# Performance work log

Measured on AMD Instinct MI355X. Metric: run time of the kernel, lower is better.

Reference implementation:

```python
import jax, jax.numpy as jnp
import numpy as np

S, B, D, H, F = 4096, 2, 512, 8, 2048
Dh = D // H
EPS = 1e-5


def _rotate_half(x):
    # matches torch: cat((-x[..., 1::2], x[..., ::2]), dim=-1)
    return jnp.concatenate([-x[..., 1::2], x[..., ::2]], axis=-1)


def _layer_norm(x, w, b):
    m = jnp.mean(x, axis=-1, keepdims=True)
    v = jnp.mean(jnp.square(x - m), axis=-1, keepdims=True)
    return (x - m) * jax.lax.rsqrt(v + EPS) * w + b


def setup_inputs() -> dict:
    key = jax.random.key(0)
    ks = jax.random.split(key, 6)
    p = lambda k, shape: (jax.random.normal(k, shape, jnp.float32) * 0.02)
    src = jax.random.normal(ks[0], (S, B, D), jnp.float32)
    # standard RoPE tables, broadcastable to [S, B, H, Dh]
    pos = jnp.arange(S, dtype=jnp.float32)
    inv_freq = 1.0 / (10000.0 ** (jnp.arange(0, Dh, 2, dtype=jnp.float32) / Dh))
    ang = pos[:, None] * inv_freq[None, :]          # [S, Dh/2]
    emb = jnp.concatenate([ang, ang], axis=-1)       # [S, Dh]
    rotary_cos = jnp.cos(emb)[:, None, None, :]
    rotary_sin = jnp.sin(emb)[:, None, None, :]
    return {
        "src": src,
        "rotary_cos": rotary_cos,
        "rotary_sin": rotary_sin,
        "in_proj_w": p(ks[1], (3 * D, D)),
        "in_proj_b": jnp.zeros((3 * D,), jnp.float32),
        "out_proj_w": p(ks[2], (D, D)),
        "out_proj_b": jnp.zeros((D,), jnp.float32),
        "w1": p(ks[3], (F, D)),
        "b1": jnp.zeros((F,), jnp.float32),
        "w2": p(ks[4], (D, F)),
        "b2": jnp.zeros((D,), jnp.float32),
        "ln1_w": jnp.ones((D,), jnp.float32),
        "ln1_b": jnp.zeros((D,), jnp.float32),
        "ln2_w": jnp.ones((D,), jnp.float32),
        "ln2_b": jnp.zeros((D,), jnp.float32),
    }


def reference(src, rotary_cos, rotary_sin, in_proj_w, in_proj_b,
              out_proj_w, out_proj_b, w1, b1, w2, b2,
              ln1_w, ln1_b, ln2_w, ln2_b):
    s = src.shape[0]
    x = _layer_norm(src, ln1_w, ln1_b)                       # [S,B,D]
    # RoPE on pre-projection tensor (q_s == k_s == x reshaped)
    xs = x.reshape(s, B, H, Dh)
    xr = (xs * rotary_cos + _rotate_half(xs) * rotary_sin).reshape(s, B, D)
    # MultiheadAttention packed in-projection
    wq, wk, wv = jnp.split(in_proj_w, 3, axis=0)
    bq, bk, bv = jnp.split(in_proj_b, 3, axis=0)
    q = (xr @ wq.T + bq).reshape(s, B, H, Dh)
    k = (xr @ wk.T + bk).reshape(s, B, H, Dh)
    v = (x @ wv.T + bv).reshape(s, B, H, Dh)
    scale = 1.0 / np.sqrt(Dh).astype(np.float32)
    scores = jnp.einsum('sbhd,tbhd->bhst', q, k) * scale     # [B,H,S,S]
    causal = jnp.triu(jnp.ones((s, s), dtype=bool), k=1)     # True = masked
    scores = jnp.where(causal, -jnp.inf, scores)
    probs = jax.nn.softmax(scores, axis=-1)
    attn = jnp.einsum('bhst,tbhd->sbhd', probs, v).reshape(s, B, D)
    attn = attn @ out_proj_w.T + out_proj_b
    src = src + attn                                         # dropout=identity (eval)
    # GELU FFN (exact erf, torch nn.GELU default)
    y = _layer_norm(src, ln2_w, ln2_b)
    y = jax.nn.gelu(y @ w1.T + b1, approximate=False) @ w2.T + b2
    return src + y
```

## Files before the change

kernel.cpp:

```cpp
#include <hip/hip_runtime.h>
#include <hip/hip_bf16.h>

typedef unsigned short u16;
typedef unsigned int u32;
using short8 = __attribute__((ext_vector_type(8))) short;
using f32x4  = __attribute__((ext_vector_type(4))) float;
using f32x16 = __attribute__((ext_vector_type(16))) float;

#define MFMA16(a,b,c) __builtin_amdgcn_mfma_f32_16x16x32_bf16((a),(b),(c),0,0,0)
#define MFMA32(a,b,c) __builtin_amdgcn_mfma_f32_32x32x16_bf16((a),(b),(c),0,0,0)
#define EXP2F(x) __builtin_amdgcn_exp2f(x)

__device__ __forceinline__ float bf2f(u16 u){
  union { u32 i; float f; } v; v.i = ((u32)u)<<16; return v.f;
}
__device__ __forceinline__ u16 f2bf(float f){
  u32 x = __float_as_uint(f);
  x += 0x7fffu + ((x>>16)&1u);
  return (u16)(x>>16);
}
__device__ __forceinline__ u32 cvtpk(float lo, float hi){
  u32 r;
  asm("v_cvt_pk_bf16_f32 %0, %1, %2" : "=v"(r) : "v"(lo), "v"(hi));
  return r;
}
__device__ __forceinline__ float cross_max(float v){
  u32 b = __float_as_uint(v);
  auto r = __builtin_amdgcn_permlane32_swap(b, b, false, false);
  return fmaxf(__uint_as_float(r[0]), __uint_as_float(r[1]));
}
__device__ __forceinline__ float cross_sum(float v){
  u32 b = __float_as_uint(v);
  auto r = __builtin_amdgcn_permlane32_swap(b, b, false, false);
  return __uint_as_float(r[0]) + __uint_as_float(r[1]);
}

typedef __attribute__((address_space(1))) const u32 GU32;
typedef __attribute__((address_space(3))) u32 LU32;
typedef __attribute__((address_space(3))) const u16 LDSU16C;
__device__ __forceinline__ void gload_lds16(const void* g, void* l){
  __builtin_amdgcn_global_load_lds((GU32*)g, (LU32*)l, 16, 0, 0);
}

template<int OFF>
__device__ __forceinline__ uint2 tr16(const u16* p){
  uint2 r;
  if constexpr (OFF == 0)
    asm volatile("ds_read_b64_tr_b16 %0, %1" : "=v"(r) : "v"((LDSU16C*)p));
  else
    asm volatile("ds_read_b64_tr_b16 %0, %1 offset:128" : "=v"(r) : "v"((LDSU16C*)p));
  return r;
}

struct ConvArgs {
  const float4* in[14];
  uint2* out[14];
  int n4[14];
  int sb[15];
};
__global__ __launch_bounds__(256)
void conv_all(ConvArgs a)
{
  int bid = blockIdx.x;
  int s = 0;
  while (s < 13 && bid >= a.sb[s+1]) ++s;
  int i = (bid - a.sb[s])*256 + threadIdx.x;
  if (i >= a.n4[s]) return;
  float4 v = a.in[s][i];
  union { uint2 u; u16 h[4]; } o;
  o.h[0] = f2bf(v.x); o.h[1] = f2bf(v.y);
  o.h[2] = f2bf(v.z); o.h[3] = f2bf(v.w);
  a.out[s][i] = o.u;
}

template<int DO_ROPE, int IN_F32>
__global__ __launch_bounds__(256)
void ln_kernel(const void* __restrict__ inv, const u16* __restrict__ lw,
               const u16* __restrict__ lb, const u16* __restrict__ ct,
               const u16* __restrict__ st, u16* __restrict__ xo,
               u16* __restrict__ xro)
{
  __shared__ float xs[4][512];
  int tid = threadIdx.x, wid = tid>>6, lane = tid&63;
  int m = blockIdx.x*4 + wid;
  int d0 = lane*8;
  float v[8], sum = 0.f, sq = 0.f;
  if (IN_F32){
    const float* in = (const float*)inv;
    float4 a = *(const float4*)(in + (size_t)m*512 + d0);
    float4 b = *(const float4*)(in + (size_t)m*512 + d0 + 4);
    v[0]=a.x; v[1]=a.y; v[2]=a.z; v[3]=a.w;
    v[4]=b.x; v[5]=b.y; v[6]=b.z; v[7]=b.w;
  } else {
    const u16* in = (const u16*)inv;
    union { uint4 q; u16 s[8]; } pk;
    pk.q = *(const uint4*)(in + (size_t)m*512 + d0);
#pragma unroll
    for (int j=0;j<8;j++) v[j] = bf2f(pk.s[j]);
  }
#pragma unroll
  for (int j=0;j<8;j++){ sum+=v[j]; sq+=v[j]*v[j]; }
#pragma unroll
  for (int o=1;o<64;o<<=1){ sum += __shfl_xor(sum,o); sq += __shfl_xor(sq,o); }
  float mean = sum*(1.f/512.f);
  float var  = sq*(1.f/512.f) - mean*mean;
  float rstd = rsqrtf(var + 1e-5f);
  float xn[8];
  union { uint4 q; u16 s[8]; } ou;
#pragma unroll
  for (int j=0;j<8;j++){
    int d = d0+j;
    xn[j] = (v[j]-mean)*rstd*bf2f(lw[d]) + bf2f(lb[d]);
    ou.s[j] = f2bf(xn[j]);
  }
  *(uint4*)(xo + (size_t)m*512 + d0) = ou.q;
  if (DO_ROPE){
#pragma unroll
    for (int j=0;j<8;j++) xs[wid][d0+j] = xn[j];
    __syncthreads();
    int si = m>>1;
    int hb = d0 & ~63;
#pragma unroll
    for (int j=0;j<8;j++){
      int d = d0+j, jh = d&63;
      float rh = (jh<32) ? -xs[wid][hb + 2*jh+1] : xs[wid][hb + 2*(jh-32)];
      float c  = bf2f(ct[si*64+jh]);
      float s2 = bf2f(st[si*64+jh]);
      ou.s[j] = f2bf(xn[j]*c + rh*s2);
    }
    *(uint4*)(xro + (size_t)m*512 + d0) = ou.q;
  }
}

#define EPI_NONE 0
#define EPI_GELU 1
#define EPI_RES  2

template<int EPI, int RES_F32, int OUT_F32, int QSCL, int SELA, int BM>
__global__ __launch_bounds__(256)
void gemm_bt(const u16* __restrict__ A, const u16* __restrict__ W,
             const u16* __restrict__ bias, const void* __restrict__ resv,
             void* __restrict__ Cv, int M, int N, int K)
{
  constexpr int IF = BM/32;
  constexpr int RF = BM/64;
  __shared__ u16 As[BM*64];
  __shared__ u16 Bs[128*64];
  int tid = threadIdx.x, wid = tid>>6, lane = tid&63;
  int l31 = lane & 31, hi = lane >> 5;
  int nbn = N >> 7;
  int bm = blockIdx.x / nbn, bn = blockIdx.x % nbn;
  int wr = wid >> 1, wc = wid & 1;
  f32x16 acc[RF][2];
#pragma unroll
  for (int i=0;i<RF;i++)
#pragma unroll
    for (int j=0;j<2;j++)
#pragma unroll
      for (int t=0;t<16;t++) acc[i][j][t] = 0.f;

  const u16* Ap = (SELA && bn >= 8) ? (const u16*)resv : A;
  const u16* Abase = Ap + (size_t)(bm*BM)*K;
  const u16* Wbase = W + (size_t)(bn*128)*K;
  int srow = lane>>3;
  int schk = ((lane&7) ^ srow) << 3;

  for (int kb = 0; kb < K; kb += 64){
#pragma unroll
    for (int i=0;i<IF;i++){
      int row = wid*(8*IF) + i*8 + srow;
      gload_lds16(Abase + (size_t)row*K + kb + schk, &As[(wid*(8*IF) + i*8)*64]);
    }
#pragma unroll
    for (int i=0;i<4;i++){
      int row = wid*32 + i*8 + srow;
      gload_lds16(Wbase + (size_t)row*K + kb + schk, &Bs[(wid*32 + i*8)*64]);
    }
    __syncthreads();
#pragma unroll
    for (int ks=0; ks<4; ++ks){
      short8 af[RF], bf8[2];
#pragma unroll
      for (int i=0;i<RF;i++){
        int row = wr*(BM/2) + i*32 + l31;
        af[i] = *(const short8*)&As[row*64 + (((2*ks + hi) ^ (row&7))<<3)];
      }
#pragma unroll
      for (int j=0;j<2;j++){
        int colr = wc*64 + j*32 + l31;
        bf8[j] = *(const short8*)&Bs[colr*64 + (((2*ks + hi) ^ (colr&7))<<3)];
      }
#pragma unroll
      for (int i=0;i<RF;i++)
#pragma unroll
        for (int j=0;j<2;j++)
          acc[i][j] = MFMA32(af[i], bf8[j], acc[i][j]);
    }
    __syncthreads();
  }
#pragma unroll
  for (int i=0;i<RF;i++){
#pragma unroll
    for (int j=0;j<2;j++){
      int col = bn*128 + wc*64 + j*32 + l31;
      float bv = bf2f(bias[col]);
#pragma unroll
      for (int t=0;t<16;t++){
        int row = bm*BM + wr*(BM/2) + i*32 + (t&3) + 8*(t>>2) + 4*hi;
        size_t idx = (size_t)row*N + col;
        float x = acc[i][j][t] + bv;
        if (EPI == EPI_GELU) x = 0.5f*x*(1.f + erff(x*0.70710678118f));
        if (EPI == EPI_RES){
          if (RES_F32) x += ((const float*)resv)[idx];
          else         x += bf2f(((const u16*)resv)[idx]);
        }
        if (QSCL && col < 512) x *= 0.18033688011f;
        if (OUT_F32) ((float*)Cv)[idx] = x;
        else         ((u16*)Cv)[idx]   = f2bf(x);
      }
    }
  }
}

__global__ __launch_bounds__(256, 3)
void attn_kernel(const u16* __restrict__ QKV, u16* __restrict__ Opart,
                 float* __restrict__ ml, u16* __restrict__ O)
{
  __shared__ u16 Ks[2][64*64];
  __shared__ u16 Vp[2][4*1024];
  int tid = threadIdx.x, wid = tid>>6, lane = tid&63;
  int l15 = lane&15, q5 = lane&31, hi = lane>>5;
  int bid = blockIdx.x;
  int qt, kt0, kt1, cid = bid;
  bool split = (bid < 768);
  if (split){
    int idx = bid >> 4;
    qt = 31 - (idx >> 1);
    int half = idx & 1;
    int nk = 2*qt + 2, h0 = nk >> 1;
    kt0 = half ? h0 : 0; kt1 = half ? nk : h0;
  } else {
    qt = 7 - ((bid - 768) >> 4);
    kt0 = 0; kt1 = 2*qt + 2;
  }
  int bh = bid & 15;
  int b = bh>>3, h = bh&7;
  size_t qkvb = (size_t)b*1536 + h*64;
  size_t vbh  = (size_t)b*512  + h*64;

  int qrow = qt*128 + wid*32 + q5;
  short8 aQ[4];
#pragma unroll
  for (int kc=0; kc<4; ++kc)
    aQ[kc] = *(const short8*)(QKV + (size_t)qrow*3072 + qkvb + 16*kc + 8*hi);

  f32x16 oacc[2];
#pragma unroll
  for (int dblk=0; dblk<2; ++dblk)
#pragma unroll
    for (int r=0;r<16;r++) oacc[dblk][r] = 0.f;
  float mrun = -3e38f, lrun = 0.f;

#define STAGE(KT, BUF)                                                              \
  {                                                                                 \
    _Pragma("unroll")                                                               \
    for (int i=0;i<2;++i){                                                          \
      gload_lds16(QKV + (size_t)((KT)*64 + wid*16 + i*8 + (lane>>3))*3072 + qkvb    \
                      + 512 + (((lane&7)^(lane>>3))<<3),                            \
                  &Ks[BUF][(wid*16 + i*8)*64]);                                     \
      int j = wid*2 + i, p = j>>1, rh = (j&1)*32;                                   \
      gload_lds16(QKV + (size_t)((KT)*64 + rh + (lane>>1))*3072 + qkvb              \
                      + 1024 + p*16 + ((lane&1)<<3),                                \
                  &Vp[BUF][p*1024 + rh*16]);                                        \
    }                                                                               \
  }

  STAGE(kt0, 0);
  int cur = 0;

  for (int kt=kt0; kt<kt1; ++kt){
    __syncthreads();
    if (kt+1 < kt1) STAGE(kt+1, cur^1);

    f32x16 sacc[2];
#pragma unroll
    for (int s=0;s<2;s++)
#pragma unroll
      for (int r=0;r<16;r++) sacc[s][r] = 0.f;
    __builtin_amdgcn_s_setprio(1);
#pragma unroll
    for (int kc=0; kc<4; ++kc)
#pragma unroll
      for (int s=0; s<2; ++s){
        int cb = (32*kc + 16*hi) ^ ((q5&7)<<4);
        short8 aK = *(const short8*)&Ks[cur][(32*s + q5)*64 + (cb>>1)];
        sacc[s] = MFMA32(aK, aQ[kc], sacc[s]);
      }
    __builtin_amdgcn_s_setprio(0);

    uint2 av[4][2][2];
#pragma unroll
    for (int kc=0; kc<4; ++kc)
#pragma unroll
      for (int dblk=0; dblk<2; ++dblk){
        const u16* base = &Vp[cur][(((lane>>4)&1) + 2*dblk)*1024 + (16*kc + 8*hi)*16 + l15*4];
        av[kc][dblk][0] = tr16<0>(base);
        av[kc][dblk][1] = tr16<128>(base);
      }

    bool diag = (kt >= 2*qt);
    float pm[4] = {-3e38f,-3e38f,-3e38f,-3e38f};
#pragma unroll
    for (int s=0;s<2;++s)
#pragma unroll
      for (int r=0;r<16;++r){
        float x = sacc[s][r];
        if (diag){
          int kv = kt*64 + 32*s + (r&3) + 8*(r>>2) + 4*hi;
          if (kv > qrow) x = -3e38f;
          sacc[s][r] = x;
        }
        pm[r&3] = fmaxf(pm[r&3], x);
      }
    float pmax = fmaxf(fmaxf(pm[0],pm[1]), fmaxf(pm[2],pm[3]));
    pmax = cross_max(pmax);
    if (!__all(pmax <= mrun + 8.f)){
      float mn = fmaxf(mrun, pmax);
      float alpha = EXP2F(mrun - mn);
      mrun = mn;
      lrun *= alpha;
#pragma unroll
      for (int dblk=0; dblk<2; ++dblk)
#pragma unroll
        for (int r=0;r<16;++r) oacc[dblk][r] *= alpha;
    }
    float ps = 0.f;
    u32 Wp[2][4][2];
#pragma unroll
    for (int s=0;s<2;++s)
#pragma unroll
      for (int p=0;p<4;++p){
        float e0 = EXP2F(sacc[s][4*p+0]-mrun);
        float e1 = EXP2F(sacc[s][4*p+1]-mrun);
        float e2 = EXP2F(sacc[s][4*p+2]-mrun);
        float e3 = EXP2F(sacc[s][4*p+3]-mrun);
        ps += (e0+e1)+(e2+e3);
        Wp[s][p][0] = cvtpk(e0,e1);
        Wp[s][p][1] = cvtpk(e2,e3);
      }
    ps = cross_sum(ps);
    lrun += ps;

    asm volatile("s_waitcnt lgkmcnt(0)");
    __builtin_amdgcn_sched_barrier(0);
    __builtin_amdgcn_s_setprio(1);
#pragma unroll
    for (int kc=0; kc<4; ++kc){
      int s = kc>>1, pA = (2*kc)&3, pB = (2*kc+1)&3;
      auto r0 = __builtin_amdgcn_permlane32_swap(Wp[s][pA][0], Wp[s][pB][0], false, false);
      auto r1 = __builtin_amdgcn_permlane32_swap(Wp[s][pA][1], Wp[s][pB][1], false, false);
      union { u32 w[4]; short8 s8; } bp;
      bp.w[0]=r0[0]; bp.w[1]=r1[0]; bp.w[2]=r0[1]; bp.w[3]=r1[1];
      union { uint2 u2[2]; short8 s8; } a0, a1;
      a0.u2[0]=av[kc][0][0]; a0.u2[1]=av[kc][0][1];
      a1.u2[0]=av[kc][1][0]; a1.u2[1]=av[kc][1][1];
      oacc[0] = MFMA32(a0.s8, bp.s8, oacc[0]);
      oacc[1] = MFMA32(a1.s8, bp.s8, oacc[1]);
    }
    __builtin_amdgcn_s_setprio(0);
    cur ^= 1;
  }

  if (split){
    u16* po = Opart + (size_t)cid*8192 + (wid*32 + q5)*64;
#pragma unroll
    for (int dblk=0; dblk<2; ++dblk)
#pragma unroll
      for (int p=0;p<4;++p){
        int d0 = 32*dblk + 8*p + 4*hi;
        union { uint2 u; u16 hh[4]; } o;
#pragma unroll
        for (int r=0;r<4;++r) o.hh[r] = f2bf(oacc[dblk][4*p+r]);
        *(uint2*)(po + d0) = o.u;
      }
    if (lane < 32){
      ml[((size_t)cid*128 + wid*32 + q5)*2 + 0] = mrun;
      ml[((size_t)cid*128 + wid*32 + q5)*2 + 1] = lrun;
    }
  } else {
    float rcp = 1.f / lrun;
#pragma unroll
    for (int dblk=0; dblk<2; ++dblk)
#pragma unroll
      for (int p=0;p<4;++p){
        int d0 = 32*dblk + 8*p + 4*hi;
        union { uint2 u; u16 hh[4]; } o;
#pragma unroll
        for (int r=0;r<4;++r) o.hh[r] = f2bf(oacc[dblk][4*p+r] * rcp);
        *(uint2*)(O + (size_t)qrow*1024 + vbh + d0) = o.u;
      }
  }
#undef STAGE
}

__global__ __launch_bounds__(128)
void attn_combine(const u16* __restrict__ Opart, const float* __restrict__ ml,
                  u16* __restrict__ O)
{
  int cb = blockIdx.x >> 4;
  int qt = 31 - cb;
  int bh = blockIdx.x & 15;
  int b = bh>>3, h = bh&7;
  int q = threadIdx.x;
  int cid0 = (cb*2)*16 + bh, cid1 = cid0 + 16;
  float m0 = ml[((size_t)cid0*128 + q)*2], l0 = ml[((size_t)cid0*128 + q)*2 + 1];
  float m1 = ml[((size_t)cid1*128 + q)*2], l1 = ml[((size_t)cid1*128 + q)*2 + 1];
  float mx = fmaxf(m0, m1);
  float w0 = EXP2F(m0 - mx), w1 = EXP2F(m1 - mx);
  float rcp = 1.f / (w0*l0 + w1*l1);
  w0 *= rcp; w1 *= rcp;
  const u16* p0 = Opart + ((size_t)cid0*128 + q)*64;
  const u16* p1 = Opart + ((size_t)cid1*128 + q)*64;
  u16* o = O + (size_t)(qt*128 + q)*1024 + b*512 + h*64;
#pragma unroll
  for (int d0=0; d0<64; d0+=8){
    union { uint4 v; u16 s[8]; } a, c, r;
    a.v = *(const uint4*)(p0 + d0);
    c.v = *(const uint4*)(p1 + d0);
#pragma unroll
    for (int j=0;j<8;j++) r.s[j] = f2bf(w0*bf2f(a.s[j]) + w1*bf2f(c.s[j]));
    *(uint4*)(o + d0) = r.v;
  }
}

extern "C" void kernel_launch(void* const* d_in, const int* in_sizes, int n_in,
                              void* d_out, int out_size, void* d_ws, size_t ws_size,
                              hipStream_t stream)
{
  float* out = (float*)d_out;
  const float* src_f = (const float*)d_in[0];
  char* ws = (char*)d_ws;
  const size_t MB = 1024ull*1024ull;
  u16* xbuf = (u16*)(ws);
  u16* xr   = (u16*)(ws +  8*MB);
  u16* qkv  = (u16*)(ws + 16*MB);
  u16* y2   = (u16*)(ws + 16*MB);
  u16* hb   = (u16*)(ws + 24*MB);
  u16* opart= (u16*)(ws + 40*MB);
  float* mlb= (float*)(ws + 52*MB);
  u16* arena= (u16*)(ws + 56*MB);
  u16* attn = xbuf;
  u16* src2 = xr;

  ConvArgs ca;
  u16* cv[15]; cv[0] = nullptr;
  {
    size_t off = 0; int blk = 0;
    for (int i=1;i<15;i++){
      cv[i] = arena + off;
      int n = in_sizes[i];
      ca.in[i-1]  = (const float4*)d_in[i];
      ca.out[i-1] = (uint2*)cv[i];
      ca.n4[i-1]  = n >> 2;
      ca.sb[i-1]  = blk;
      blk += ((n>>2) + 255) / 256;
      off += (size_t)n;
    }
    ca.sb[14] = blk;
    conv_all<<<blk, 256, 0, stream>>>(ca);
  }
  const u16* rcos = cv[1];
  const u16* rsin = cv[2];
  const u16* inw  = cv[3];
  const u16* inb  = cv[4];
  const u16* outw = cv[5];
  const u16* outb = cv[6];
  const u16* w1   = cv[7];
  const u16* b1   = cv[8];
  const u16* w2   = cv[9];
  const u16* b2   = cv[10];
  const u16* ln1w = cv[11];
  const u16* ln1b = cv[12];
  const u16* ln2w = cv[13];
  const u16* ln2b = cv[14];

  ln_kernel<1,1><<<2048, 256, 0, stream>>>(src_f, ln1w, ln1b, rcos, rsin, xbuf, xr);

  gemm_bt<EPI_NONE,0,0,1,1,128><<<768, 256, 0, stream>>>(xr, inw, inb, xbuf, qkv, 8192, 1536, 512);

  attn_kernel<<<896, 256, 0, stream>>>(qkv, opart, mlb, attn);
  attn_combine<<<384, 128, 0, stream>>>(opart, mlb, attn);

  gemm_bt<EPI_RES,1,0,0,0,64><<<512, 256, 0, stream>>>(attn, outw, outb, src_f, src2, 8192, 512, 512);

  ln_kernel<0,0><<<2048, 256, 0, stream>>>(src2, ln2w, ln2b, nullptr, nullptr, y2, nullptr);

  gemm_bt<EPI_GELU,0,0,0,0,128><<<1024, 256, 0, stream>>>(y2, w1, b1, nullptr, hb, 8192, 2048, 512);
  gemm_bt<EPI_RES,0,1,0,0,64><<<512, 256, 0, stream>>>(hb, w2, b2, src2, out, 8192, 512, 2048);
}
```

Baseline: 195.0 us.

## Double-buffer LDS tiles in GEMM to overlap global loads with MFMA

Splits the A and W shared-memory tiles into two buffers. The loads for the next K-slice are issued right after the barrier, while the MFMAs run on the current buffer, which removes the second barrier per iteration. The aim is to hide global-to-LDS load latency behind the math. In exchange it doubles the shared-memory footprint, which can lower occupancy, and it depends on the barrier waiting for the outstanding direct-to-LDS loads.

```diff
diff --git a/kernel.cpp b/kernel.cpp
--- a/kernel.cpp
+++ b/kernel.cpp
@@ -144,8 +144,8 @@
 {
   constexpr int IF = BM/32;
   constexpr int RF = BM/64;
-  __shared__ u16 As[BM*64];
-  __shared__ u16 Bs[128*64];
+  __shared__ u16 As[2][BM*64];
+  __shared__ u16 Bs[2][128*64];
   int tid = threadIdx.x, wid = tid>>6, lane = tid&63;
   int l31 = lane & 31, hi = lane >> 5;
   int nbn = N >> 7;
@@ -165,30 +165,40 @@
   int srow = lane>>3;
   int schk = ((lane&7) ^ srow) << 3;
 
+#define GSTAGE(KB, BUF)                                                          \
+  {                                                                              \
+    _Pragma("unroll")                                                            \
+    for (int i=0;i<IF;i++){                                                      \
+      int row = wid*(8*IF) + i*8 + srow;                                         \
+      gload_lds16(Abase + (size_t)row*K + (KB) + schk,                           \
+                  &As[BUF][(wid*(8*IF) + i*8)*64]);                              \
+    }                                                                            \
+    _Pragma("unroll")                                                            \
+    for (int i=0;i<4;i++){                                                       \
+      int row = wid*32 + i*8 + srow;                                             \
+      gload_lds16(Wbase + (size_t)row*K + (KB) + schk,                           \
+                  &Bs[BUF][(wid*32 + i*8)*64]);                                  \
+    }                                                                            \
+  }
+
+  GSTAGE(0, 0);
+  int cur = 0;
+
   for (int kb = 0; kb < K; kb += 64){
-#pragma unroll
-    for (int i=0;i<IF;i++){
-      int row = wid*(8*IF) + i*8 + srow;
-      gload_lds16(Abase + (size_t)row*K + kb + schk, &As[(wid*(8*IF) + i*8)*64]);
-    }
-#pragma unroll
-    for (int i=0;i<4;i++){
-      int row = wid*32 + i*8 + srow;
-      gload_lds16(Wbase + (size_t)row*K + kb + schk, &Bs[(wid*32 + i*8)*64]);
-    }
     __syncthreads();
+    if (kb + 64 < K) GSTAGE(kb + 64, cur^1);
 #pragma unroll
     for (int ks=0; ks<4; ++ks){
       short8 af[RF], bf8[2];
 #pragma unroll
       for (int i=0;i<RF;i++){
         int row = wr*(BM/2) + i*32 + l31;
-        af[i] = *(const short8*)&As[row*64 + (((2*ks + hi) ^ (row&7))<<3)];
+        af[i] = *(const short8*)&As[cur][row*64 + (((2*ks + hi) ^ (row&7))<<3)];
       }
 #pragma unroll
       for (int j=0;j<2;j++){
         int colr = wc*64 + j*32 + l31;
-        bf8[j] = *(const short8*)&Bs[colr*64 + (((2*ks + hi) ^ (colr&7))<<3)];
+        bf8[j] = *(const short8*)&Bs[cur][colr*64 + (((2*ks + hi) ^ (colr&7))<<3)];
       }
 #pragma unroll
       for (int i=0;i<RF;i++)
@@ -196,8 +206,9 @@
         for (int j=0;j<2;j++)
           acc[i][j] = MFMA32(af[i], bf8[j], acc[i][j]);
     }
-    __syncthreads();
-  }
+    cur ^= 1;
+  }
+#undef GSTAGE
 #pragma unroll
   for (int i=0;i<RF;i++){
 #pragma unroll
```

New measurement: 200.8 us. 3.0% more time.
